# Performance work log

Hardware: AMD Instinct MI355X
Metric: run time of the kernel (lower is better)

The kernel has to match this reference:

```python
import jax, jax.numpy as jnp
import numpy as np
import math

SAMPLE_RATIO = 0.25
K = 5
EPS = 1e-6

def _cells(loc_orig, H, W):
    # map normalized [-1,1] coords to nearest grid cell index, as in tcformer token2map/map2token
    loc = jnp.clip(loc_orig, -1.0, 1.0)
    px = jnp.clip(jnp.round(0.5 * (loc[..., 0] + 1.0) * W - 0.5).astype(jnp.int32), 0, W - 1)
    py = jnp.clip(jnp.round(0.5 * (loc[..., 1] + 1.0) * H - 0.5).astype(jnp.int32), 0, H - 1)
    return py * W + px  # [B, N0]

def token2map(x, loc_orig, idx_agg, H, W):
    B, N, C = x.shape
    N0 = loc_orig.shape[1]
    cell = _cells(loc_orig, H, W)
    seg = (cell + jnp.arange(B)[:, None] * (H * W)).reshape(-1)
    feat = x[jnp.arange(B)[:, None], idx_agg]  # [B, N0, C] token feature per original point
    sums = jax.ops.segment_sum(feat.reshape(-1, C), seg, num_segments=B * H * W)
    cnt = jax.ops.segment_sum(jnp.ones((B * N0,), x.dtype), seg, num_segments=B * H * W)
    x_map = sums / (cnt[:, None] + EPS)  # per-cell mean over points hitting the cell
    return x_map.reshape(B, H, W, C).transpose(0, 3, 1, 2)

def map2token(x_map, N, loc_orig, idx_agg, agg_weight):
    B, C, H, W = x_map.shape
    cell = _cells(loc_orig, H, W)
    val = x_map.reshape(B, C, H * W).transpose(0, 2, 1)  # [B, HW, C]
    vpt = val[jnp.arange(B)[:, None], cell]              # [B, N0, C] map value at each point
    seg = (idx_agg + jnp.arange(B)[:, None] * N).reshape(-1)
    w = agg_weight.reshape(-1)
    wsum = jax.ops.segment_sum(w, seg, num_segments=B * N) + EPS
    ssum = jax.ops.segment_sum(vpt.reshape(-1, C) * w[:, None], seg, num_segments=B * N)
    return (ssum / wsum[:, None]).reshape(B, N, C)  # agg_weight-weighted mean per token

def token_cluster_merge(x, Ns, idx_agg, weight, k):
    B, N, C = x.shape
    # DPC-KNN clustering (index computation; mirrors torch.no_grad block)
    sq = jnp.sum(x * x, -1)
    d2 = jnp.clip(sq[:, :, None] + sq[:, None, :] - 2.0 * jnp.einsum('bnc,bmc->bnm', x, x), 0.0, None)
    dist = jnp.sqrt(d2) / (C ** 0.5)
    dnear = -jax.lax.top_k(-dist, k)[0]                  # k smallest distances (incl. self)
    density = jnp.exp(-jnp.mean(dnear * dnear, -1))
    mask = density[:, None, :] > density[:, :, None]
    dmax = jnp.max(dist.reshape(B, -1), -1)[:, None, None]
    parent_dist = jnp.min(jnp.where(mask, dist, dmax), -1)  # dist to nearest higher-density token
    score = parent_dist * density
    index_down = jax.lax.top_k(score, Ns)[1]             # [B, Ns] cluster centers
    idx_cluster = jnp.argmin(dist[jnp.arange(B)[:, None], index_down], axis=1)  # [B, N]
    idx_cluster = idx_cluster.at[jnp.arange(B)[:, None], index_down].set(jnp.arange(Ns)[None, :])
    # weighted merge of tokens into clusters
    seg = (idx_cluster + jnp.arange(B)[:, None] * Ns).reshape(-1)
    w = weight.reshape(-1)
    allw = jax.ops.segment_sum(w, seg, num_segments=B * Ns) + EPS
    norm_w = (w / allw[seg]).reshape(B, N)
    x_merged = jax.ops.segment_sum((x * norm_w[:, :, None]).reshape(-1, C), seg, num_segments=B * Ns).reshape(B, Ns, C)
    idx_agg_down = idx_cluster[jnp.arange(B)[:, None], idx_agg]      # compose index maps
    weight_t = norm_w[jnp.arange(B)[:, None], idx_agg][..., None]    # [B, N0, 1]
    return x_merged, idx_agg_down, weight_t

def _forward(x, loc_orig, idx_agg, agg_weight, idx_k_loc, H, W, conv_w, conv_b, skip_w, ln_g, ln_b, conf_w, conf_b):
    B, N, C = x.shape
    x_map = token2map(x, loc_orig, idx_agg, H, W)
    x_map = jax.lax.conv_general_dilated(x_map, conv_w, (2, 2), ((1, 1), (1, 1))) + conv_b[None, :, None, None]
    x_tok = map2token(x_map, N, loc_orig, idx_agg, agg_weight) + jnp.einsum('bnc,oc->bno', x, skip_w)
    mu = jnp.mean(x_tok, -1, keepdims=True)
    var = jnp.mean((x_tok - mu) ** 2, -1, keepdims=True)
    x_tok = (x_tok - mu) / jnp.sqrt(var + 1e-5) * ln_g + ln_b
    conf = jnp.einsum('bnc,oc->bno', x_tok, conf_w) + conf_b
    weight = jnp.exp(conf)
    Ns = max(math.ceil(N * SAMPLE_RATIO), 1)
    x_down, idx_agg_down, weight_t = token_cluster_merge(x_tok, Ns, idx_agg, weight, K)
    agg_weight_down = agg_weight * weight_t
    agg_weight_down = agg_weight_down / jnp.max(agg_weight_down, axis=1, keepdims=True)
    # down_block is an injected submodule; treated as identity passthrough here
    return x_down, idx_agg_down, agg_weight_down

def setup_inputs():
    key = jax.random.key(0)
    ks = jax.random.split(key, 8)
    B, N, C, N0, Cout = 8, 256, 256, 16384, 512
    return {
        'x': jax.random.normal(ks[0], (B, N, C), jnp.float32),
        'loc_orig': jax.random.uniform(ks[1], (B, N0, 2), jnp.float32, -1.0, 1.0),
        'idx_agg': jax.random.randint(ks[2], (B, N0), 0, N),
        'agg_weight': jax.random.uniform(ks[3], (B, N0, 1), jnp.float32, 0.1, 1.0),
        'idx_k_loc': jax.random.randint(ks[4], (B, N0, K), 0, N0),
        'H': 64, 'W': 64,
        'conv_w': jax.random.normal(ks[5], (Cout, C, 3, 3), jnp.float32) * 0.02,
        'conv_b': jnp.zeros((Cout,), jnp.float32),
        'skip_w': jax.random.normal(ks[6], (Cout, C), jnp.float32) * 0.02,
        'ln_g': jnp.ones((Cout,), jnp.float32),
        'ln_b': jnp.zeros((Cout,), jnp.float32),
        'conf_w': jax.random.normal(ks[7], (1, Cout), jnp.float32) * 0.02,
        'conf_b': jnp.zeros((1,), jnp.float32),
    }

def reference(x, loc_orig, idx_agg, agg_weight, idx_k_loc, H, W, conv_w, conv_b, skip_w, ln_g, ln_b, conf_w, conf_b):
    return _forward(x, loc_orig, idx_agg, agg_weight, idx_k_loc, H, W, conv_w, conv_b, skip_w, ln_g, ln_b, conf_w, conf_b)
```

## Files before the change

### kernel.cpp

```cpp
#include <hip/hip_runtime.h>
#include <math.h>

typedef unsigned long long ull;
typedef __attribute__((ext_vector_type(8))) short short8v;
typedef __attribute__((ext_vector_type(4))) float float4v;

#define NB   8
#define NTOK 256
#define CIN  256
#define NP   16384
#define NCO  512
#define HW64 4096
#define OHW  1024
#define NS   64
#define EPS  1e-6f
#define KC   2304
#define NKC  72

constexpr size_t OFF_SUMS = 0;
constexpr size_t OFF_CNT  = OFF_SUMS + (size_t)NB*HW64*CIN;
constexpr size_t OFF_AMAT = OFF_CNT  + (size_t)NB*HW64;
constexpr size_t OFF_ALLW = OFF_AMAT + (size_t)NB*NTOK*OHW;
constexpr size_t OFF_DMAX = OFF_ALLW + (size_t)NB*NS;
constexpr size_t OFF_MAXW = OFF_DMAX + NB;
constexpr size_t ZERO_END = OFF_MAXW + NB;
constexpr size_t OFF_WT   = ZERO_END;
constexpr size_t OFF_SKWT = OFF_WT   + (size_t)KC*NCO;
constexpr size_t OFF_Y    = OFF_SKWT + (size_t)CIN*NCO;
constexpr size_t OFF_C2   = OFF_Y    + (size_t)NB*OHW*NCO;
constexpr size_t OFF_WSUM = OFF_C2   + (size_t)NB*NTOK*NCO;
constexpr size_t OFF_XSKIP= OFF_WSUM + (size_t)NB*NTOK;
constexpr size_t OFF_XTOK = OFF_XSKIP+ (size_t)NB*NTOK*NCO;
constexpr size_t OFF_XPK  = OFF_XTOK + (size_t)NB*NTOK*NCO;
constexpr size_t OFF_WEXP = OFF_XPK  + (size_t)NB*NTOK*NCO;
constexpr size_t OFF_SQ   = OFF_WEXP + (size_t)NB*NTOK;
constexpr size_t OFF_DIST = OFF_SQ   + (size_t)NB*NTOK;
constexpr size_t OFF_DENS = OFF_DIST + (size_t)NB*NTOK*NTOK;
constexpr size_t OFF_SCORE= OFF_DENS + (size_t)NB*NTOK;
constexpr size_t OFF_IND  = OFF_SCORE+ (size_t)NB*NTOK;
constexpr size_t OFF_IDXCL= OFF_IND  + (size_t)NB*NS;
constexpr size_t OFF_NORMW= OFF_IDXCL+ (size_t)NB*NTOK;
constexpr size_t OFF_AWBUF= OFF_NORMW+ (size_t)NB*NTOK;
constexpr size_t OFF_XTPK = OFF_AWBUF+ (size_t)NB*NP;
constexpr size_t OFF_XTOKPK= OFF_Y;

__device__ __forceinline__ unsigned pack_hl(float x) {
    unsigned u = __float_as_uint(x);
    unsigned t = u + 0x7fffu + ((u >> 16) & 1u);
    unsigned hibits = t & 0xffff0000u;
    float lo = x - __uint_as_float(hibits);
    unsigned ul = __float_as_uint(lo);
    unsigned lt = ul + 0x7fffu + ((ul >> 16) & 1u);
    return hibits | (lt >> 16);
}
__device__ __forceinline__ unsigned f2bf(float f) {
    unsigned u = __float_as_uint(f);
    return (u + 0x7fffu + ((u >> 16) & 1u)) >> 16;
}
__device__ __forceinline__ unsigned hp2(unsigned w0, unsigned w1) {
    return __builtin_amdgcn_perm(w1, w0, 0x07060302u);
}
__device__ __forceinline__ unsigned lp2(unsigned w0, unsigned w1) {
    return __builtin_amdgcn_perm(w1, w0, 0x05040100u);
}

__global__ void hist(const float* __restrict__ loc, const int* __restrict__ idxagg,
                     const float* __restrict__ aggw,
                     int* __restrict__ cntmat, float* __restrict__ cnt,
                     float* __restrict__ amat) {
    int bp = blockIdx.x*256 + threadIdx.x;
    int b  = bp >> 14;
    float lx = loc[2*bp+0], ly = loc[2*bp+1];
    lx = fminf(fmaxf(lx, -1.f), 1.f);
    ly = fminf(fmaxf(ly, -1.f), 1.f);
    int px = (int)rintf((lx + 1.f)*32.f - 0.5f); px = min(max(px,0),63);
    int py = (int)rintf((ly + 1.f)*32.f - 0.5f); py = min(max(py,0),63);
    int cell = py*64 + px;
    int tok = idxagg[bp];
    atomicAdd(&cntmat[((size_t)(b*HW64 + cell))*NTOK + tok], 1);
    atomicAdd(&cnt[b*HW64 + cell], 1.0f);
    int qx = (int)rintf((lx + 1.f)*16.f - 0.5f); qx = min(max(qx,0),31);
    int qy = (int)rintf((ly + 1.f)*16.f - 0.5f); qy = min(max(qy,0),31);
    atomicAdd(&amat[((size_t)(b*NTOK + tok))*OHW + qy*32 + qx], aggw[bp]);
}

__global__ void prep_pack(const float* __restrict__ x, unsigned* __restrict__ xtpk,
                          unsigned* __restrict__ xpk,
                          const float* __restrict__ convw, uint4* __restrict__ wtf,
                          const float4* __restrict__ skipw, uint4* __restrict__ skwt) {
    int blk = blockIdx.x;
    if (blk < 2048) {
        int id = blk*256 + threadIdx.x;
        int tok = id & 255, cin = (id >> 8) & 255, b = id >> 16;
        unsigned pk = pack_hl(x[((size_t)(b*NTOK + tok))*CIN + cin]);
        xtpk[id] = pk;
        xpk[((size_t)(b*NTOK + tok))*CIN + cin] = pk;
    } else if (blk < 3200) {
        int tid = (blk - 2048)*256 + threadIdx.x;
        int lane = tid & 63;
        int r1 = tid >> 6;
        int h = r1 & 1;
        int r2 = r1 >> 1;
        int f = r2 & 3;
        int r3 = r2 >> 2;
        int kc = r3 % NKC, mt = r3 / NKC;
        int cout = mt*64 + f*16 + (lane & 15);
        int kb = kc*32 + (lane >> 4)*8;
        unsigned s[8];
        #pragma unroll
        for (int j = 0; j < 8; ++j) {
            int k = kb + j;
            int grp = k >> 8, cin = k & 255;
            unsigned w = pack_hl(convw[(size_t)cout*KC + cin*9 + grp]);
            s[j] = h ? (w & 0xffffu) : (w >> 16);
        }
        uint4 o;
        o.x = s[0] | (s[1]<<16); o.y = s[2] | (s[3]<<16);
        o.z = s[4] | (s[5]<<16); o.w = s[6] | (s[7]<<16);
        wtf[tid] = o;
    } else {
        size_t i = (size_t)(blk - 3200)*256 + threadIdx.x;
        float4 v = skipw[i];
        uint4 o;
        o.x = pack_hl(v.x); o.y = pack_hl(v.y); o.z = pack_hl(v.z); o.w = pack_hl(v.w);
        skwt[i] = o;
    }
}

__launch_bounds__(512)
__global__ void map_gemm(const int* __restrict__ A, const unsigned* __restrict__ B,
                         const float* __restrict__ cnt, unsigned* __restrict__ xmapu) {
    __shared__ __align__(16) unsigned short Ah[4096];
    __shared__ __align__(16) unsigned short Bh[8192], Bl[8192];
    int z = blockIdx.z, m0 = blockIdx.y*128;
    const int* Ab = A + ((size_t)z*HW64 + m0)*NTOK;
    const unsigned* Bb = B + (size_t)z*CIN*NTOK;
    int t = threadIdx.x, lane = t & 63;
    int w = t >> 6;
    int wm = w >> 2, wn = w & 3;
    int l15 = lane & 15, l4 = lane >> 4;
    int rowA = t & 127, kgA = t >> 7;
    int rowB = t & 255, kgB0 = (t >> 8)*2;
    const int* arow = Ab + (size_t)rowA*NTOK + kgA*8;
    const unsigned* brow = Bb + (size_t)rowB*NTOK + kgB0*8;
    int wbA = (rowA>>4)*512 + kgA*128 + (rowA&15)*8;
    int wbB = (rowB>>4)*512 + kgB0*128 + (rowB&15)*8;

    float4v acc[4][4] = {};
    int4 ia0, ia1;
    uint4 rb[2][2];
    auto loadA = [&](int kc) {
        const int* p = arow + kc*32;
        ia0 = *(const int4*)p; ia1 = *(const int4*)(p + 4);
    };
    auto loadB = [&](int kc) {
        #pragma unroll
        for (int s = 0; s < 2; ++s) {
            const unsigned* p = brow + kc*32 + s*8;
            rb[s][0] = *(const uint4*)p; rb[s][1] = *(const uint4*)(p + 4);
        }
    };
    loadA(0); loadB(0);

    for (int kc = 0; kc < 8; ++kc) {
        __syncthreads();
        uint4 h, l;
        h.x = f2bf((float)ia0.x) | (f2bf((float)ia0.y) << 16);
        h.y = f2bf((float)ia0.z) | (f2bf((float)ia0.w) << 16);
        h.z = f2bf((float)ia1.x) | (f2bf((float)ia1.y) << 16);
        h.w = f2bf((float)ia1.z) | (f2bf((float)ia1.w) << 16);
        *(uint4*)&Ah[wbA] = h;
        #pragma unroll
        for (int s = 0; s < 2; ++s) {
            uint4 u0 = rb[s][0], u1 = rb[s][1];
            h.x=hp2(u0.x,u0.y); h.y=hp2(u0.z,u0.w); h.z=hp2(u1.x,u1.y); h.w=hp2(u1.z,u1.w);
            l.x=lp2(u0.x,u0.y); l.y=lp2(u0.z,u0.w); l.z=lp2(u1.x,u1.y); l.w=lp2(u1.z,u1.w);
            *(uint4*)&Bh[wbB + s*128] = h; *(uint4*)&Bl[wbB + s*128] = l;
        }
        __syncthreads();
        if (kc < 7) { loadA(kc+1); loadB(kc+1); }

        short8v bh[4], bl[4];
        #pragma unroll
        for (int q = 0; q < 4; ++q) {
            int off = (wn*4 + q)*512 + l4*128 + l15*8;
            bh[q] = *(const short8v*)&Bh[off];
            bl[q] = *(const short8v*)&Bl[off];
        }
        #pragma unroll
        for (int p = 0; p < 4; ++p) {
            int off = (wm*4 + p)*512 + l4*128 + l15*8;
            short8v ah = *(const short8v*)&Ah[off];
            #pragma unroll
            for (int q = 0; q < 4; ++q) {
                acc[p][q] = __builtin_amdgcn_mfma_f32_16x16x32_bf16(ah, bh[q], acc[p][q], 0, 0, 0);
                acc[p][q] = __builtin_amdgcn_mfma_f32_16x16x32_bf16(ah, bl[q], acc[p][q], 0, 0, 0);
            }
        }
    }

    const float* cntb = cnt + (size_t)z*HW64;
    #pragma unroll
    for (int p = 0; p < 4; ++p) {
        int mb = m0 + wm*64 + p*16 + l4*4;
        #pragma unroll
        for (int q = 0; q < 4; ++q) {
            int n = wn*64 + q*16 + l15;
            #pragma unroll
            for (int r = 0; r < 4; ++r) {
                float v = acc[p][q][r] / (cntb[mb + r] + EPS);
                xmapu[((size_t)z*HW64 + mb + r)*CIN + n] = pack_hl(v);
            }
        }
    }
}

__launch_bounds__(256)
__global__ void conv_gemm(const unsigned* __restrict__ xmap, const uint4* __restrict__ wtf,
                          const float* __restrict__ convb, unsigned* __restrict__ ytp) {
    __shared__ __align__(16) unsigned short Ahi[2][4096], Alo[2][4096];
    int n0 = blockIdx.x * 128;
    int mt = blockIdx.y;
    int m0 = mt * 64;
    int t = threadIdx.x;
    int lane = t & 63, wid = t >> 6;
    int wm = wid >> 1, wn = wid & 1;
    int l15 = lane & 15, l4 = lane >> 4;

    int rowL = t & 127, kg = t >> 7;
    int posG = n0 + rowL;
    int bb = posG >> 10, rem = posG & 1023;
    int oy = rem >> 5, ox = rem & 31;

    int wbA0 = (rowL>>4)*512 + kg*128 + (rowL&15)*8;
    int wbA1 = wbA0 + 256;

    float4v acc[4][2] = {};
    uint4 aA0,aA1,aA2,aA3;
    uint4 aB0,aB1,aB2,aB3;

    auto addrA = [&](int kc, int* ok) -> const unsigned* {
        int grp = kc >> 3;
        int ky = grp/3, kx = grp - 3*ky;
        int iy = 2*oy - 1 + ky, ix = 2*ox - 1 + kx;
        *ok = ((unsigned)iy < 64u) && ((unsigned)ix < 64u);
        return xmap + ((((size_t)bb*64 + iy)*64 + ix)*256 + (kc&7)*32 + kg*8);
    };
    auto loadA_A = [&](int kc) {
        int ok; const unsigned* ap = addrA(kc, &ok);
        if (ok) {
            aA0 = *(const uint4*)ap;       aA1 = *(const uint4*)(ap + 4);
            aA2 = *(const uint4*)(ap + 16); aA3 = *(const uint4*)(ap + 20);
        } else { aA0 = make_uint4(0,0,0,0); aA1 = aA0; aA2 = aA0; aA3 = aA0; }
    };
    auto loadA_B = [&](int kc) {
        int ok; const unsigned* ap = addrA(kc, &ok);
        if (ok) {
            aB0 = *(const uint4*)ap;       aB1 = *(const uint4*)(ap + 4);
            aB2 = *(const uint4*)(ap + 16); aB3 = *(const uint4*)(ap + 20);
        } else { aB0 = make_uint4(0,0,0,0); aB1 = aB0; aB2 = aB0; aB3 = aB0; }
    };
    auto repack_A = [&](int buf) {
        uint4 h, l;
        h.x=hp2(aA0.x,aA0.y); h.y=hp2(aA0.z,aA0.w); h.z=hp2(aA1.x,aA1.y); h.w=hp2(aA1.z,aA1.w);
        l.x=lp2(aA0.x,aA0.y); l.y=lp2(aA0.z,aA0.w); l.z=lp2(aA1.x,aA1.y); l.w=lp2(aA1.z,aA1.w);
        *(uint4*)&Ahi[buf][wbA0] = h; *(uint4*)&Alo[buf][wbA0] = l;
        h.x=hp2(aA2.x,aA2.y); h.y=hp2(aA2.z,aA2.w); h.z=hp2(aA3.x,aA3.y); h.w=hp2(aA3.z,aA3.w);
        l.x=lp2(aA2.x,aA2.y); l.y=lp2(aA2.z,aA2.w); l.z=lp2(aA3.x,aA3.y); l.w=lp2(aA3.z,aA3.w);
        *(uint4*)&Ahi[buf][wbA1] = h; *(uint4*)&Alo[buf][wbA1] = l;
    };
    auto repack_B = [&](int buf) {
        uint4 h, l;
        h.x=hp2(aB0.x,aB0.y); h.y=hp2(aB0.z,aB0.w); h.z=hp2(aB1.x,aB1.y); h.w=hp2(aB1.z,aB1.w);
        l.x=lp2(aB0.x,aB0.y); l.y=lp2(aB0.z,aB0.w); l.z=lp2(aB1.x,aB1.y); l.w=lp2(aB1.z,aB1.w);
        *(uint4*)&Ahi[buf][wbA0] = h; *(uint4*)&Alo[buf][wbA0] = l;
        h.x=hp2(aB2.x,aB2.y); h.y=hp2(aB2.z,aB2.w); h.z=hp2(aB3.x,aB3.y); h.w=hp2(aB3.z,aB3.w);
        l.x=lp2(aB2.x,aB2.y); l.y=lp2(aB2.z,aB2.w); l.z=lp2(aB3.x,aB3.y); l.w=lp2(aB3.z,aB3.w);
        *(uint4*)&Ahi[buf][wbA1] = h; *(uint4*)&Alo[buf][wbA1] = l;
    };
    const uint4* wbase = wtf + ((size_t)(((mt*NKC)*4 + wn*2)*2))*64 + lane;

    short8v bhc[2], blc[2], bhn[2], bln[2];
    #pragma unroll
    for (int q = 0; q < 2; ++q) {
        bhc[q] = *(const short8v*)(wbase + q*128);
        blc[q] = *(const short8v*)(wbase + q*128 + 64);
    }
    loadA_B(0);
    repack_B(0);
    loadA_A(1);
    __syncthreads();
    int cur = 0;

    #define CONV_MFMA_BLOCK                                                            \
        _Pragma("unroll")                                                              \
        for (int p = 0; p < 4; ++p) {                                                  \
            int off = (wm*4 + p)*512 + l4*128 + l15*8;                                 \
            short8v ah = *(const short8v*)&Ahi[cur][off];                              \
            short8v al = *(const short8v*)&Alo[cur][off];                              \
            _Pragma("unroll")                                                          \
            for (int q = 0; q < 2; ++q) {                                              \
                acc[p][q] = __builtin_amdgcn_mfma_f32_16x16x32_bf16(ah, bhc[q], acc[p][q], 0, 0, 0); \
                acc[p][q] = __builtin_amdgcn_mfma_f32_16x16x32_bf16(ah, blc[q], acc[p][q], 0, 0, 0); \
                acc[p][q] = __builtin_amdgcn_mfma_f32_16x16x32_bf16(al, bhc[q], acc[p][q], 0, 0, 0); \
            }                                                                          \
        }

    for (int kc = 0; kc < NKC; kc += 2) {
        {
            const uint4* wb = wbase + (size_t)(kc+1)*512;
            #pragma unroll
            for (int q = 0; q < 2; ++q) {
                bhn[q] = *(const short8v*)(wb + q*128);
                bln[q] = *(const short8v*)(wb + q*128 + 64);
            }
        }
        if (kc + 2 < NKC) loadA_B(kc + 2);
        CONV_MFMA_BLOCK
        repack_A(cur ^ 1);
        #pragma unroll
        for (int q = 0; q < 2; ++q) { bhc[q] = bhn[q]; blc[q] = bln[q]; }
        __syncthreads();
        cur ^= 1;

        int k1 = kc + 1;
        if (k1 + 1 < NKC) {
            const uint4* wb = wbase + (size_t)(k1+1)*512;
            #pragma unroll
            for (int q = 0; q < 2; ++q) {
                bhn[q] = *(const short8v*)(wb + q*128);
                bln[q] = *(const short8v*)(wb + q*128 + 64);
            }
        }
        if (k1 + 2 < NKC) loadA_A(k1 + 2);
        CONV_MFMA_BLOCK
        if (k1 + 1 < NKC) {
            repack_B(cur ^ 1);
            #pragma unroll
            for (int q = 0; q < 2; ++q) { bhc[q] = bhn[q]; blc[q] = bln[q]; }
        }
        __syncthreads();
        cur ^= 1;
    }
    #undef CONV_MFMA_BLOCK

    int bbk = n0 >> 10;
    int pos0 = (n0 & 1023) + wm*64;
    #pragma unroll
    for (int p = 0; p < 4; ++p) {
        int posb = pos0 + p*16 + l4*4;
        #pragma unroll
        for (int q = 0; q < 2; ++q) {
            int col = m0 + wn*32 + q*16 + l15;
            float bv = convb[col];
            uint4 o;
            o.x = pack_hl(acc[p][q][0] + bv);
            o.y = pack_hl(acc[p][q][1] + bv);
            o.z = pack_hl(acc[p][q][2] + bv);
            o.w = pack_hl(acc[p][q][3] + bv);
            *(uint4*)&ytp[((size_t)(bbk*NCO + col))*OHW + posb] = o;
        }
    }
}

template<int MODE, int TM, int TN, int AF>
__launch_bounds__(256)
__global__ void gemm_pk(const void* __restrict__ Av, const unsigned* __restrict__ B,
                        float* __restrict__ C, int K, int N,
                        long sA, long sB, long sC,
                        const float* __restrict__ aux, unsigned* __restrict__ dmaxU) {
    constexpr int NA = TM/64, NBs = TN/64;
    constexpr int WSM = TM/64;
    constexpr int WSN = 4/WSM;
    constexpr int TWM = TM/WSM, TWN = TN/WSN;
    constexpr int P = TWM/16, Q = TWN/16;
    __shared__ __align__(16) unsigned short Ahi[TM*32], Alo[TM*32];
    __shared__ __align__(16) unsigned short Bhi[TN*32], Blo[TN*32];
    int z = blockIdx.z;
    const unsigned* Ab = (const unsigned*)Av + (size_t)z*sA;
    const unsigned* Bb = B + (size_t)z*sB;
    float* Cb = C + (size_t)z*sC;
    int n0 = blockIdx.x*TN, m0 = blockIdx.y*TM;
    int t = threadIdx.x;
    int lane = t & 63, wid = t >> 6;
    int wm = (WSM==2) ? (wid >> 1) : 0;
    int wn = (WSM==2) ? (wid & 1)  : wid;
    int l15 = lane & 15, l4 = lane >> 4;

    int rowA = t & (TM-1), kgA = t / TM;
    int rowB = t & (TN-1), kgB = t / TN;
    const unsigned* arow = Ab + (size_t)(m0 + rowA)*K + kgA*8;
    const unsigned* brw  = Bb + (size_t)(n0 + rowB)*K + kgB*8;
    int wbA = (rowA>>4)*512 + kgA*128 + (rowA&15)*8;
    int wbB = (rowB>>4)*512 + kgB*128 + (rowB&15)*8;

    float4v acc[P][Q] = {};
    uint4 ra[NA][2], rb[NBs][2];
    auto loadA = [&](int kc) {
        #pragma unroll
        for (int s = 0; s < NA; ++s) {
            const unsigned* p = arow + (size_t)kc*32 + s*16;
            ra[s][0] = *(const uint4*)p; ra[s][1] = *(const uint4*)(p + 4);
        }
    };
    auto loadB = [&](int kc) {
        #pragma unroll
        for (int s = 0; s < NBs; ++s) {
            const unsigned* p = brw + (size_t)kc*32 + s*16;
            rb[s][0] = *(const uint4*)p; rb[s][1] = *(const uint4*)(p + 4);
        }
    };
    loadA(0); loadB(0);
    int nkc = K >> 5;

    for (int kc = 0; kc < nkc; ++kc) {
        __syncthreads();
        uint4 h, l;
        #pragma unroll
        for (int s = 0; s < NA; ++s) {
            uint4 u0 = ra[s][0], u1 = ra[s][1];
            if (AF == 0) {
                h.x=hp2(u0.x,u0.y); h.y=hp2(u0.z,u0.w); h.z=hp2(u1.x,u1.y); h.w=hp2(u1.z,u1.w);
                l.x=lp2(u0.x,u0.y); l.y=lp2(u0.z,u0.w); l.z=lp2(u1.x,u1.y); l.w=lp2(u1.z,u1.w);
            } else {
                unsigned pk0 = pack_hl(__uint_as_float(u0.x)), pk1 = pack_hl(__uint_as_float(u0.y));
                unsigned pk2 = pack_hl(__uint_as_float(u0.z)), pk3 = pack_hl(__uint_as_float(u0.w));
                unsigned pk4 = pack_hl(__uint_as_float(u1.x)), pk5 = pack_hl(__uint_as_float(u1.y));
                unsigned pk6 = pack_hl(__uint_as_float(u1.z)), pk7 = pack_hl(__uint_as_float(u1.w));
                h.x = (pk0>>16) | (pk1 & 0xffff0000u); h.y = (pk2>>16) | (pk3 & 0xffff0000u);
                h.z = (pk4>>16) | (pk5 & 0xffff0000u); h.w = (pk6>>16) | (pk7 & 0xffff0000u);
                l.x = (pk0&0xffffu) | (pk1<<16); l.y = (pk2&0xffffu) | (pk3<<16);
                l.z = (pk4&0xffffu) | (pk5<<16); l.w = (pk6&0xffffu) | (pk7<<16);
            }
            *(uint4*)&Ahi[wbA + s*256] = h; *(uint4*)&Alo[wbA + s*256] = l;
        }
        #pragma unroll
        for (int s = 0; s < NBs; ++s) {
            uint4 u0 = rb[s][0], u1 = rb[s][1];
            h.x=hp2(u0.x,u0.y); h.y=hp2(u0.z,u0.w); h.z=hp2(u1.x,u1.y); h.w=hp2(u1.z,u1.w);
            l.x=lp2(u0.x,u0.y); l.y=lp2(u0.z,u0.w); l.z=lp2(u1.x,u1.y); l.w=lp2(u1.z,u1.w);
            *(uint4*)&Bhi[wbB + s*256] = h; *(uint4*)&Blo[wbB + s*256] = l;
        }
        __syncthreads();
        if (kc + 1 < nkc) { loadA(kc+1); loadB(kc+1); }

        short8v bh[Q], bl[Q];
        #pragma unroll
        for (int q = 0; q < Q; ++q) {
            int off = (wn*Q + q)*512 + l4*128 + l15*8;
            bh[q] = *(const short8v*)&Bhi[off];
            bl[q] = *(const short8v*)&Blo[off];
        }
        #pragma unroll
        for (int p = 0; p < P; ++p) {
            int off = (wm*P + p)*512 + l4*128 + l15*8;
            short8v ah = *(const short8v*)&Ahi[off];
            short8v al = *(const short8v*)&Alo[off];
            #pragma unroll
            for (int q = 0; q < Q; ++q) {
                acc[p][q] = __builtin_amdgcn_mfma_f32_16x16x32_bf16(ah, bh[q], acc[p][q], 0, 0, 0);
                acc[p][q] = __builtin_amdgcn_mfma_f32_16x16x32_bf16(ah, bl[q], acc[p][q], 0, 0, 0);
                acc[p][q] = __builtin_amdgcn_mfma_f32_16x16x32_bf16(al, bh[q], acc[p][q], 0, 0, 0);
            }
        }
    }

    if (MODE == 0) {
        #pragma unroll
        for (int p = 0; p < P; ++p) {
            int mb = m0 + wm*TWM + p*16 + l4*4;
            #pragma unroll
            for (int q = 0; q < Q; ++q) {
                int n = n0 + wn*TWN + q*16 + l15;
                #pragma unroll
                for (int r = 0; r < 4; ++r)
                    Cb[(size_t)(mb + r)*N + n] = acc[p][q][r];
            }
        }
    } else {
        const float inv = 1.0f / sqrtf(512.0f);
        const float* sqb = aux + (size_t)z*NTOK;
        float tmax = 0.f;
        #pragma unroll
        for (int p = 0; p < P; ++p) {
            int mb = m0 + wm*TWM + p*16 + l4*4;
            #pragma unroll
            for (int q = 0; q < Q; ++q) {
                int n = n0 + wn*TWN + q*16 + l15;
                float sn = sqb[n];
                #pragma unroll
                for (int r = 0; r < 4; ++r) {
                    float d2 = sqb[mb + r] + sn - 2.0f*acc[p][q][r];
                    float d = sqrtf(fmaxf(d2, 0.0f)) * inv;
                    Cb[(size_t)(mb + r)*N + n] = d;
                    tmax = fmaxf(tmax, d);
                }
            }
        }
        __shared__ float redm[4];
        #pragma unroll
        for (int off = 32; off; off >>= 1) tmax = fmaxf(tmax, __shfl_xor(tmax, off, 64));
        if (lane == 0) redm[wid] = tmax;
        __syncthreads();
        if (t == 0) {
            float m = fmaxf(fmaxf(redm[0], redm[1]), fmaxf(redm[2], redm[3]));
            atomicMax(dmaxU + z, __float_as_uint(m));
        }
    }
}

__global__ void wsum_rows(const float* __restrict__ amat, float* __restrict__ wsum) {
    int row = blockIdx.x*4 + (threadIdx.x >> 6);
    int lane = threadIdx.x & 63;
    const float* ar = amat + (size_t)row*OHW;
    float s = 0.f;
    #pragma unroll
    for (int r = 0; r < 16; ++r) s += ar[lane + 64*r];
    #pragma unroll
    for (int off = 32; off; off >>= 1) s += __shfl_xor(s, off, 64);
    if (lane == 0) wsum[row] = s;
}

__device__ __forceinline__ float block_sum256(float v, float* red) {
    #pragma unroll
    for (int off = 32; off; off >>= 1) v += __shfl_xor(v, off, 64);
    __syncthreads();
    if ((threadIdx.x & 63) == 0) red[threadIdx.x >> 6] = v;
    __syncthreads();
    return red[0] + red[1] + red[2] + red[3];
}

__global__ void ln_conf(const float* __restrict__ C2, const float* __restrict__ wsum,
                        const float* __restrict__ xskip, const float* __restrict__ g,
                        const float* __restrict__ be, const float* __restrict__ confw,
                        const float* __restrict__ confb, float* __restrict__ xtok,
                        unsigned* __restrict__ xtokpk,
                        float* __restrict__ wexp, float* __restrict__ sqv) {
    __shared__ float red[4];
    int row = blockIdx.x, t = threadIdx.x;
    float ws = wsum[row] + EPS;
    size_t base = (size_t)row*NCO;
    float v0 = C2[base + t]       / ws + xskip[base + t];
    float v1 = C2[base + t + 256] / ws + xskip[base + t + 256];
    float mu  = block_sum256(v0 + v1, red) / 512.0f;
    float d0 = v0 - mu, d1 = v1 - mu;
    float var = block_sum256(d0*d0 + d1*d1, red) / 512.0f;
    float sv = sqrtf(var + 1e-5f);
    float x0 = d0/sv * g[t]       + be[t];
    float x1 = d1/sv * g[t + 256] + be[t + 256];
    xtok[base + t] = x0;
    xtok[base + t + 256] = x1;
    xtokpk[base + t] = pack_hl(x0);
    xtokpk[base + t + 256] = pack_hl(x1);
    float cs = block_sum256(x0*confw[t] + x1*confw[t + 256], red);
    float qs = block_sum256(x0*x0 + x1*x1, red);
    if (t == 0) {
        wexp[row] = expf(cs + confb[0]);
        sqv[row]  = qs;
    }
}

__global__ void knn_dens(const float* __restrict__ dist, float* __restrict__ dens) {
    int row = blockIdx.x*4 + (threadIdx.x >> 6);
    int lane = threadIdx.x & 63;
    const float* dr = dist + (size_t)row*NTOK;
    float v0 = dr[lane], v1 = dr[lane+64], v2 = dr[lane+128], v3 = dr[lane+192];
    float acc = 0.f;
    #pragma unroll
    for (int it = 0; it < 5; ++it) {
        float lm = fminf(fminf(v0, v1), fminf(v2, v3));
        float gm = lm;
        #pragma unroll
        for (int off = 32; off; off >>= 1) gm = fminf(gm, __shfl_xor(gm, off, 64));
        acc += gm*gm;
        ull ball = __ballot(lm == gm);
        int first = __ffsll(ball) - 1;
        if (lane == first) {
            if      (v0 == gm) v0 = 1e30f;
            else if (v1 == gm) v1 = 1e30f;
            else if (v2 == gm) v2 = 1e30f;
            else               v3 = 1e30f;
        }
    }
    if (lane == 0) dens[row] = expf(-(acc/5.0f));
}

__global__ void parent_score(const float* __restrict__ dist, const float* __restrict__ dens,
                             const unsigned* __restrict__ dmaxU, float* __restrict__ score) {
    int row = blockIdx.x*4 + (threadIdx.x >> 6);
    int lane = threadIdx.x & 63;
    int b = row >> 8;
    float di = dens[row];
    float dm = __uint_as_float(dmaxU[b]);
    const float* dr = dist + (size_t)row*NTOK;
    const float* db = dens + (size_t)b*NTOK;
    float pd = dm;
    #pragma unroll
    for (int r = 0; r < 4; ++r) {
        int j = lane + 64*r;
        pd = fminf(pd, (db[j] > di) ? dr[j] : dm);
    }
    #pragma unroll
    for (int off = 32; off; off >>= 1) pd = fminf(pd, __shfl_xor(pd, off, 64));
    if (lane == 0) score[row] = pd * di;
}

__global__ void topk64(const float* __restrict__ score, int* __restrict__ ind) {
    int b = blockIdx.x, lane = threadIdx.x;
    const float* sb = score + b*NTOK;
    ull k0, k1, k2, k3;
    {
        unsigned i0 = lane, i1 = lane+64, i2 = lane+128, i3 = lane+192;
        k0 = ((ull)(__float_as_uint(sb[i0]) + 1u) << 32) | (unsigned)(4095 - i0);
        k1 = ((ull)(__float_as_uint(sb[i1]) + 1u) << 32) | (unsigned)(4095 - i1);
        k2 = ((ull)(__float_as_uint(sb[i2]) + 1u) << 32) | (unsigned)(4095 - i2);
        k3 = ((ull)(__float_as_uint(sb[i3]) + 1u) << 32) | (unsigned)(4095 - i3);
    }
    for (int it = 0; it < 64; ++it) {
        ull lm = k0;
        if (k1 > lm) lm = k1;
        if (k2 > lm) lm = k2;
        if (k3 > lm) lm = k3;
        ull gm = lm;
        #pragma unroll
        for (int off = 32; off; off >>= 1) {
            ull o = __shfl_xor(gm, off, 64);
            if (o > gm) gm = o;
        }
        if (lane == 0) ind[b*NS + it] = 4095 - (int)(gm & 0xffffffffull);
        if      (k0 == gm) k0 = 0;
        else if (k1 == gm) k1 = 0;
        else if (k2 == gm) k2 = 0;
        else if (k3 == gm) k3 = 0;
    }
}

__global__ void assign_k(const float* __restrict__ dist, const int* __restrict__ ind,
                         int* __restrict__ idxcl) {
    int row = blockIdx.x*4 + (threadIdx.x >> 6);
    int lane = threadIdx.x & 63;
    int b = row >> 8, i = row & 255;
    int center = ind[b*NS + lane];
    float d = dist[((size_t)(b*NTOK + center))*NTOK + i];
    ull key = ((ull)__float_as_uint(d) << 32) | (unsigned)lane;
    #pragma unroll
    for (int off = 32; off; off >>= 1) {
        ull o = __shfl_xor(key, off, 64);
        if (o < key) key = o;
    }
    if (lane == 0) idxcl[row] = (int)(key & 0xffffffffull);
}

__global__ void finalize_cl(const int* __restrict__ ind, const float* __restrict__ wexp,
                            int* __restrict__ idxcl, float* __restrict__ normw) {
    __shared__ float allwL[NS];
    int b = blockIdx.x, t = threadIdx.x;
    if (t < NS) {
        idxcl[b*NTOK + ind[b*NS + t]] = t;
        allwL[t] = 0.f;
    }
    __syncthreads();
    int cl = idxcl[b*NTOK + t];
    float we = wexp[b*NTOK + t];
    atomicAdd(&allwL[cl], we);
    __syncthreads();
    normw[b*NTOK + t] = we / (allwL[cl] + EPS);
}

__global__ void merge_k(const float* __restrict__ xtok, const int* __restrict__ idxcl,
                        const float* __restrict__ normw, float* __restrict__ xout) {
    int row = blockIdx.x, t = threadIdx.x;
    int b = row >> 8;
    int cl = idxcl[row];
    float nw = normw[row];
    float* o = xout + ((size_t)(b*NS + cl))*NCO;
    const float* xr = xtok + (size_t)row*NCO;
    atomicAdd(&o[t],       xr[t]       * nw);
    atomicAdd(&o[t + 256], xr[t + 256] * nw);
}

__global__ void out_idx_aw(const int* __restrict__ idxagg, const float* __restrict__ aggw,
                           const int* __restrict__ idxcl, const float* __restrict__ normw,
                           float* __restrict__ dout, float* __restrict__ awbuf,
                           unsigned* __restrict__ maxw) {
    __shared__ float red[4];
    int bp = blockIdx.x*256 + threadIdx.x;
    int b = bp >> 14;
    int tok = idxagg[bp];
    int cl = idxcl[b*NTOK + tok];
    dout[(size_t)NB*NS*NCO + bp] = (float)cl;
    float aw = aggw[bp] * normw[b*NTOK + tok];
    awbuf[bp] = aw;
    float m = aw;
    #pragma unroll
    for (int off = 32; off; off >>= 1) m = fmaxf(m, __shfl_xor(m, off, 64));
    if ((threadIdx.x & 63) == 0) red[threadIdx.x >> 6] = m;
    __syncthreads();
    if (threadIdx.x == 0) {
        float mm = fmaxf(fmaxf(red[0], red[1]), fmaxf(red[2], red[3]));
        atomicMax(&maxw[b], __float_as_uint(mm));
    }
}

__global__ void aw_final(const float* __restrict__ awbuf, const float* __restrict__ maxw,
                         float* __restrict__ dout) {
    int bp = blockIdx.x*256 + threadIdx.x;
    int b = bp >> 14;
    dout[(size_t)NB*NS*NCO + (size_t)NB*NP + bp] = awbuf[bp] / maxw[b];
}

extern "C" void kernel_launch(void* const* d_in, const int* in_sizes, int n_in,
                              void* d_out, int out_size, void* d_ws, size_t ws_size,
                              hipStream_t stream) {
    const float* x      = (const float*)d_in[0];
    const float* loc    = (const float*)d_in[1];
    const int*   idxagg = (const int*)  d_in[2];
    const float* aggw   = (const float*)d_in[3];
    const float* convw  = (const float*)d_in[7];
    const float* convb  = (const float*)d_in[8];
    const float* skipw  = (const float*)d_in[9];
    const float* lng    = (const float*)d_in[10];
    const float* lnb    = (const float*)d_in[11];
    const float* confw  = (const float*)d_in[12];
    const float* confb  = (const float*)d_in[13];

    float* ws = (float*)d_ws;
    float* dout = (float*)d_out;

    (void)hipMemsetAsync(ws, 0, ZERO_END*sizeof(float), stream);
    (void)hipMemsetAsync(dout, 0, (size_t)NB*NS*NCO*sizeof(float), stream);

    hist<<<dim3(NB*NP/256), 256, 0, stream>>>(loc, idxagg, aggw,
                                              (int*)(ws + OFF_SUMS), ws + OFF_CNT, ws + OFF_AMAT);
    prep_pack<<<dim3(3328), 256, 0, stream>>>(x, (unsigned*)(ws + OFF_XTPK),
                                              (unsigned*)(ws + OFF_XPK),
                                              convw, (uint4*)(ws + OFF_WT),
                                              (const float4*)skipw, (uint4*)(ws + OFF_SKWT));

    map_gemm<<<dim3(1, 32, 8), 512, 0, stream>>>((const int*)(ws + OFF_SUMS),
                                                 (const unsigned*)(ws + OFF_XTPK),
                                                 ws + OFF_CNT,
                                                 (unsigned*)(ws + OFF_SUMS));

    conv_gemm<<<dim3(64, 8), 256, 0, stream>>>((const unsigned*)(ws + OFF_SUMS),
                                               (const uint4*)(ws + OFF_WT), convb,
                                               (unsigned*)(ws + OFF_Y));

    wsum_rows<<<dim3(NB*NTOK/4), 256, 0, stream>>>(ws + OFF_AMAT, ws + OFF_WSUM);
    gemm_pk<0,64,64,1><<<dim3(8, 4, 8), 256, 0, stream>>>((const void*)(ws + OFF_AMAT),
                                                  (const unsigned*)(ws + OFF_Y),
                                                  ws + OFF_C2, OHW, NCO,
                                                  (long)NTOK*OHW, (long)NCO*OHW, (long)NTOK*NCO,
                                                  nullptr, nullptr);
    gemm_pk<0,64,64,0><<<dim3(8, 32, 1), 256, 0, stream>>>((const void*)(ws + OFF_XPK),
                                                   (const unsigned*)(ws + OFF_SKWT),
                                                   ws + OFF_XSKIP, CIN, NCO, 0, 0, 0,
                                                   nullptr, nullptr);

    ln_conf<<<dim3(NB*NTOK), 256, 0, stream>>>(ws + OFF_C2, ws + OFF_WSUM, ws + OFF_XSKIP,
                                               lng, lnb, confw, confb,
                                               ws + OFF_XTOK, (unsigned*)(ws + OFF_XTOKPK),
                                               ws + OFF_WEXP, ws + OFF_SQ);

    gemm_pk<1,64,64,0><<<dim3(4, 4, 8), 256, 0, stream>>>((const void*)(ws + OFF_XTOKPK),
                                                  (const unsigned*)(ws + OFF_XTOKPK),
                                                  ws + OFF_DIST, NCO, NTOK,
                                                  (long)NTOK*NCO, (long)NTOK*NCO, (long)NTOK*NTOK,
                                                  ws + OFF_SQ, (unsigned*)(ws + OFF_DMAX));

    knn_dens<<<dim3(NB*NTOK/4), 256, 0, stream>>>(ws + OFF_DIST, ws + OFF_DENS);
    parent_score<<<dim3(NB*NTOK/4), 256, 0, stream>>>(ws + OFF_DIST, ws + OFF_DENS,
                                                      (const unsigned*)(ws + OFF_DMAX), ws + OFF_SCORE);
    topk64<<<dim3(NB), 64, 0, stream>>>(ws + OFF_SCORE, (int*)(ws + OFF_IND));
    assign_k<<<dim3(NB*NTOK/4), 256, 0, stream>>>(ws + OFF_DIST, (const int*)(ws + OFF_IND),
                                                  (int*)(ws + OFF_IDXCL));
    finalize_cl<<<dim3(NB), 256, 0, stream>>>((const int*)(ws + OFF_IND), ws + OFF_WEXP,
                                              (int*)(ws + OFF_IDXCL), ws + OFF_NORMW);

    merge_k<<<dim3(NB*NTOK), 256, 0, stream>>>(ws + OFF_XTOK, (const int*)(ws + OFF_IDXCL),
                                               ws + OFF_NORMW, dout);
    out_idx_aw<<<dim3(NB*NP/256), 256, 0, stream>>>(idxagg, aggw, (const int*)(ws + OFF_IDXCL),
                                                    ws + OFF_NORMW, dout, ws + OFF_AWBUF,
                                                    (unsigned*)(ws + OFF_MAXW));
    aw_final<<<dim3(NB*NP/256), 256, 0, stream>>>(ws + OFF_AWBUF, (const float*)(ws + OFF_MAXW), dout);
}
```

Before: 282.1 us.

## Pack histogram counts into 16-bit pairs and double conv K-stage size

The per-cell token count matrix is stored as two packed 16-bit counters per word. It lives in the Y buffer region, so the count matrix and the memset that clears it are half the size, and map_gemm reads half the bytes for A. The conv GEMM now stages 64 channels per LDS buffer instead of 32, which halves the number of barriers and repack rounds per K loop at the cost of twice the shared memory and more staging registers. Packed counters assume no cell/token pair exceeds 65535 hits, which holds here since each batch has at most 16384 points.

Result: slower. 296.7 us (+5.2%).

```diff
diff --git a/kernel.cpp b/kernel.cpp
--- a/kernel.cpp
+++ b/kernel.cpp
@@ -16,6 +16,7 @@
 #define EPS  1e-6f
 #define KC   2304
 #define NKC  72
+#define NPAIR 36
 
 constexpr size_t OFF_SUMS = 0;
 constexpr size_t OFF_CNT  = OFF_SUMS + (size_t)NB*HW64*CIN;
@@ -66,7 +67,7 @@
 
 __global__ void hist(const float* __restrict__ loc, const int* __restrict__ idxagg,
                      const float* __restrict__ aggw,
-                     int* __restrict__ cntmat, float* __restrict__ cnt,
+                     unsigned* __restrict__ cnt16, float* __restrict__ cnt,
                      float* __restrict__ amat) {
     int bp = blockIdx.x*256 + threadIdx.x;
     int b  = bp >> 14;
@@ -77,7 +78,7 @@
     int py = (int)rintf((ly + 1.f)*32.f - 0.5f); py = min(max(py,0),63);
     int cell = py*64 + px;
     int tok = idxagg[bp];
-    atomicAdd(&cntmat[((size_t)(b*HW64 + cell))*NTOK + tok], 1);
+    atomicAdd(&cnt16[((size_t)(b*HW64 + cell))*128 + (tok >> 1)], 1u << ((tok & 1)*16));
     atomicAdd(&cnt[b*HW64 + cell], 1.0f);
     int qx = (int)rintf((lx + 1.f)*16.f - 0.5f); qx = min(max(qx,0),31);
     int qy = (int)rintf((ly + 1.f)*16.f - 0.5f); qy = min(max(qy,0),31);
@@ -128,12 +129,12 @@
 }
 
 __launch_bounds__(512)
-__global__ void map_gemm(const int* __restrict__ A, const unsigned* __restrict__ B,
+__global__ void map_gemm(const unsigned* __restrict__ A16, const unsigned* __restrict__ B,
                          const float* __restrict__ cnt, unsigned* __restrict__ xmapu) {
     __shared__ __align__(16) unsigned short Ah[4096];
     __shared__ __align__(16) unsigned short Bh[8192], Bl[8192];
     int z = blockIdx.z, m0 = blockIdx.y*128;
-    const int* Ab = A + ((size_t)z*HW64 + m0)*NTOK;
+    const unsigned* Ab = A16 + ((size_t)z*HW64 + m0)*128;
     const unsigned* Bb = B + (size_t)z*CIN*NTOK;
     int t = threadIdx.x, lane = t & 63;
     int w = t >> 6;
@@ -141,17 +142,16 @@
     int l15 = lane & 15, l4 = lane >> 4;
     int rowA = t & 127, kgA = t >> 7;
     int rowB = t & 255, kgB0 = (t >> 8)*2;
-    const int* arow = Ab + (size_t)rowA*NTOK + kgA*8;
+    const unsigned* arow = Ab + (size_t)rowA*128 + kgA*4;
     const unsigned* brow = Bb + (size_t)rowB*NTOK + kgB0*8;
     int wbA = (rowA>>4)*512 + kgA*128 + (rowA&15)*8;
     int wbB = (rowB>>4)*512 + kgB0*128 + (rowB&15)*8;
 
     float4v acc[4][4] = {};
-    int4 ia0, ia1;
+    uint4 ia;
     uint4 rb[2][2];
     auto loadA = [&](int kc) {
-        const int* p = arow + kc*32;
-        ia0 = *(const int4*)p; ia1 = *(const int4*)(p + 4);
+        ia = *(const uint4*)(arow + kc*16);
     };
     auto loadB = [&](int kc) {
         #pragma unroll
@@ -165,10 +165,10 @@
     for (int kc = 0; kc < 8; ++kc) {
         __syncthreads();
         uint4 h, l;
-        h.x = f2bf((float)ia0.x) | (f2bf((float)ia0.y) << 16);
-        h.y = f2bf((float)ia0.z) | (f2bf((float)ia0.w) << 16);
-        h.z = f2bf((float)ia1.x) | (f2bf((float)ia1.y) << 16);
-        h.w = f2bf((float)ia1.z) | (f2bf((float)ia1.w) << 16);
+        h.x = f2bf((float)(ia.x & 0xffffu)) | (f2bf((float)(ia.x >> 16)) << 16);
+        h.y = f2bf((float)(ia.y & 0xffffu)) | (f2bf((float)(ia.y >> 16)) << 16);
+        h.z = f2bf((float)(ia.z & 0xffffu)) | (f2bf((float)(ia.z >> 16)) << 16);
+        h.w = f2bf((float)(ia.w & 0xffffu)) | (f2bf((float)(ia.w >> 16)) << 16);
         *(uint4*)&Ah[wbA] = h;
         #pragma unroll
         for (int s = 0; s < 2; ++s) {
@@ -218,7 +218,7 @@
 __launch_bounds__(256)
 __global__ void conv_gemm(const unsigned* __restrict__ xmap, const uint4* __restrict__ wtf,
                           const float* __restrict__ convb, unsigned* __restrict__ ytp) {
-    __shared__ __align__(16) unsigned short Ahi[2][4096], Alo[2][4096];
+    __shared__ __align__(16) unsigned short Ahi[2][8192], Alo[2][8192];
     int n0 = blockIdx.x * 128;
     int mt = blockIdx.y;
     int m0 = mt * 64;
@@ -231,118 +231,125 @@
     int posG = n0 + rowL;
     int bb = posG >> 10, rem = posG & 1023;
     int oy = rem >> 5, ox = rem & 31;
-
-    int wbA0 = (rowL>>4)*512 + kg*128 + (rowL&15)*8;
-    int wbA1 = wbA0 + 256;
+    int wbBase = (rowL>>4)*1024 + (kg*4)*128 + (rowL&15)*8;
 
     float4v acc[4][2] = {};
-    uint4 aA0,aA1,aA2,aA3;
-    uint4 aB0,aB1,aB2,aB3;
-
-    auto addrA = [&](int kc, int* ok) -> const unsigned* {
-        int grp = kc >> 3;
+    uint4 rA[8], rB[8];
+
+    auto stageA = [&](int pr) {
+        int grp = pr >> 2;
         int ky = grp/3, kx = grp - 3*ky;
         int iy = 2*oy - 1 + ky, ix = 2*ox - 1 + kx;
-        *ok = ((unsigned)iy < 64u) && ((unsigned)ix < 64u);
-        return xmap + ((((size_t)bb*64 + iy)*64 + ix)*256 + (kc&7)*32 + kg*8);
+        if ((unsigned)iy < 64u && (unsigned)ix < 64u) {
+            const unsigned* ap = xmap + ((((size_t)bb*64 + iy)*64 + ix)*256 + (pr&3)*64 + kg*32);
+            #pragma unroll
+            for (int s = 0; s < 8; ++s) rA[s] = *(const uint4*)(ap + s*4);
+        } else {
+            #pragma unroll
+            for (int s = 0; s < 8; ++s) rA[s] = make_uint4(0,0,0,0);
+        }
     };
-    auto loadA_A = [&](int kc) {
-        int ok; const unsigned* ap = addrA(kc, &ok);
-        if (ok) {
-            aA0 = *(const uint4*)ap;       aA1 = *(const uint4*)(ap + 4);
-            aA2 = *(const uint4*)(ap + 16); aA3 = *(const uint4*)(ap + 20);
-        } else { aA0 = make_uint4(0,0,0,0); aA1 = aA0; aA2 = aA0; aA3 = aA0; }
+    auto stageB = [&](int pr) {
+        int grp = pr >> 2;
+        int ky = grp/3, kx = grp - 3*ky;
+        int iy = 2*oy - 1 + ky, ix = 2*ox - 1 + kx;
+        if ((unsigned)iy < 64u && (unsigned)ix < 64u) {
+            const unsigned* ap = xmap + ((((size_t)bb*64 + iy)*64 + ix)*256 + (pr&3)*64 + kg*32);
+            #pragma unroll
+            for (int s = 0; s < 8; ++s) rB[s] = *(const uint4*)(ap + s*4);
+        } else {
+            #pragma unroll
+            for (int s = 0; s < 8; ++s) rB[s] = make_uint4(0,0,0,0);
+        }
     };
-    auto loadA_B = [&](int kc) {
-        int ok; const unsigned* ap = addrA(kc, &ok);
-        if (ok) {
-            aB0 = *(const uint4*)ap;       aB1 = *(const uint4*)(ap + 4);
-            aB2 = *(const uint4*)(ap + 16); aB3 = *(const uint4*)(ap + 20);
-        } else { aB0 = make_uint4(0,0,0,0); aB1 = aB0; aB2 = aB0; aB3 = aB0; }
+    auto repackA = [&](int buf) {
+        #pragma unroll
+        for (int s = 0; s < 4; ++s) {
+            uint4 u0 = rA[2*s], u1 = rA[2*s+1], h, l;
+            h.x=hp2(u0.x,u0.y); h.y=hp2(u0.z,u0.w); h.z=hp2(u1.x,u1.y); h.w=hp2(u1.z,u1.w);
+            l.x=lp2(u0.x,u0.y); l.y=lp2(u0.z,u0.w); l.z=lp2(u1.x,u1.y); l.w=lp2(u1.z,u1.w);
+            *(uint4*)&Ahi[buf][wbBase + s*128] = h;
+            *(uint4*)&Alo[buf][wbBase + s*128] = l;
+        }
     };
-    auto repack_A = [&](int buf) {
-        uint4 h, l;
-        h.x=hp2(aA0.x,aA0.y); h.y=hp2(aA0.z,aA0.w); h.z=hp2(aA1.x,aA1.y); h.w=hp2(aA1.z,aA1.w);
-        l.x=lp2(aA0.x,aA0.y); l.y=lp2(aA0.z,aA0.w); l.z=lp2(aA1.x,aA1.y); l.w=lp2(aA1.z,aA1.w);
-        *(uint4*)&Ahi[buf][wbA0] = h; *(uint4*)&Alo[buf][wbA0] = l;
-        h.x=hp2(aA2.x,aA2.y); h.y=hp2(aA2.z,aA2.w); h.z=hp2(aA3.x,aA3.y); h.w=hp2(aA3.z,aA3.w);
-        l.x=lp2(aA2.x,aA2.y); l.y=lp2(aA2.z,aA2.w); l.z=lp2(aA3.x,aA3.y); l.w=lp2(aA3.z,aA3.w);
-        *(uint4*)&Ahi[buf][wbA1] = h; *(uint4*)&Alo[buf][wbA1] = l;
-    };
-    auto repack_B = [&](int buf) {
-        uint4 h, l;
-        h.x=hp2(aB0.x,aB0.y); h.y=hp2(aB0.z,aB0.w); h.z=hp2(aB1.x,aB1.y); h.w=hp2(aB1.z,aB1.w);
-        l.x=lp2(aB0.x,aB0.y); l.y=lp2(aB0.z,aB0.w); l.z=lp2(aB1.x,aB1.y); l.w=lp2(aB1.z,aB1.w);
-        *(uint4*)&Ahi[buf][wbA0] = h; *(uint4*)&Alo[buf][wbA0] = l;
-        h.x=hp2(aB2.x,aB2.y); h.y=hp2(aB2.z,aB2.w); h.z=hp2(aB3.x,aB3.y); h.w=hp2(aB3.z,aB3.w);
-        l.x=lp2(aB2.x,aB2.y); l.y=lp2(aB2.z,aB2.w); l.z=lp2(aB3.x,aB3.y); l.w=lp2(aB3.z,aB3.w);
-        *(uint4*)&Ahi[buf][wbA1] = h; *(uint4*)&Alo[buf][wbA1] = l;
+    auto repackB = [&](int buf) {
+        #pragma unroll
+        for (int s = 0; s < 4; ++s) {
+            uint4 u0 = rB[2*s], u1 = rB[2*s+1], h, l;
+            h.x=hp2(u0.x,u0.y); h.y=hp2(u0.z,u0.w); h.z=hp2(u1.x,u1.y); h.w=hp2(u1.z,u1.w);
+            l.x=lp2(u0.x,u0.y); l.y=lp2(u0.z,u0.w); l.z=lp2(u1.x,u1.y); l.w=lp2(u1.z,u1.w);
+            *(uint4*)&Ahi[buf][wbBase + s*128] = h;
+            *(uint4*)&Alo[buf][wbBase + s*128] = l;
+        }
     };
     const uint4* wbase = wtf + ((size_t)(((mt*NKC)*4 + wn*2)*2))*64 + lane;
 
     short8v bhc[2], blc[2], bhn[2], bln[2];
+    #define LOADB(kc)                                                   \
+        {                                                               \
+            const uint4* wb = wbase + (size_t)(kc)*512;                 \
+            _Pragma("unroll")                                           \
+            for (int q = 0; q < 2; ++q) {                               \
+                bhn[q] = *(const short8v*)(wb + q*128);                 \
+                bln[q] = *(const short8v*)(wb + q*128 + 64);            \
+            }                                                           \
+        }
+    #define BSWAP                                                       \
+        _Pragma("unroll")                                               \
+        for (int q = 0; q < 2; ++q) { bhc[q] = bhn[q]; blc[q] = bln[q]; }
+
+    #define CONV_MFMA(J)                                                                    \
+        _Pragma("unroll")                                                                   \
+        for (int p = 0; p < 4; ++p) {                                                       \
+            int off = (wm*4 + p)*1024 + ((J)*4 + l4)*128 + l15*8;                           \
+            short8v ah = *(const short8v*)&Ahi[cur][off];                                   \
+            short8v al = *(const short8v*)&Alo[cur][off];                                   \
+            _Pragma("unroll")                                                               \
+            for (int q = 0; q < 2; ++q) {                                                   \
+                acc[p][q] = __builtin_amdgcn_mfma_f32_16x16x32_bf16(ah, bhc[q], acc[p][q], 0, 0, 0); \
+                acc[p][q] = __builtin_amdgcn_mfma_f32_16x16x32_bf16(ah, blc[q], acc[p][q], 0, 0, 0); \
+                acc[p][q] = __builtin_amdgcn_mfma_f32_16x16x32_bf16(al, bhc[q], acc[p][q], 0, 0, 0); \
+            }                                                                               \
+        }
+
+    stageB(0);
+    repackB(0);
     #pragma unroll
     for (int q = 0; q < 2; ++q) {
         bhc[q] = *(const short8v*)(wbase + q*128);
         blc[q] = *(const short8v*)(wbase + q*128 + 64);
     }
-    loadA_B(0);
-    repack_B(0);
-    loadA_A(1);
+    stageA(1);
     __syncthreads();
     int cur = 0;
 
-    #define CONV_MFMA_BLOCK                                                            \
-        _Pragma("unroll")                                                              \
-        for (int p = 0; p < 4; ++p) {                                                  \
-            int off = (wm*4 + p)*512 + l4*128 + l15*8;                                 \
-            short8v ah = *(const short8v*)&Ahi[cur][off];                              \
-            short8v al = *(const short8v*)&Alo[cur][off];                              \
-            _Pragma("unroll")                                                          \
-            for (int q = 0; q < 2; ++q) {                                              \
-                acc[p][q] = __builtin_amdgcn_mfma_f32_16x16x32_bf16(ah, bhc[q], acc[p][q], 0, 0, 0); \
-                acc[p][q] = __builtin_amdgcn_mfma_f32_16x16x32_bf16(ah, blc[q], acc[p][q], 0, 0, 0); \
-                acc[p][q] = __builtin_amdgcn_mfma_f32_16x16x32_bf16(al, bhc[q], acc[p][q], 0, 0, 0); \
-            }                                                                          \
-        }
-
-    for (int kc = 0; kc < NKC; kc += 2) {
-        {
-            const uint4* wb = wbase + (size_t)(kc+1)*512;
-            #pragma unroll
-            for (int q = 0; q < 2; ++q) {
-                bhn[q] = *(const short8v*)(wb + q*128);
-                bln[q] = *(const short8v*)(wb + q*128 + 64);
-            }
-        }
-        if (kc + 2 < NKC) loadA_B(kc + 2);
-        CONV_MFMA_BLOCK
-        repack_A(cur ^ 1);
-        #pragma unroll
-        for (int q = 0; q < 2; ++q) { bhc[q] = bhn[q]; blc[q] = bln[q]; }
+    for (int pr = 0; pr < NPAIR; pr += 2) {
+        LOADB(2*pr + 1);
+        if (pr + 2 < NPAIR) stageB(pr + 2);
+        CONV_MFMA(0)
+        BSWAP
+        LOADB(2*pr + 2);
+        CONV_MFMA(1)
+        repackA(cur ^ 1);
+        BSWAP
         __syncthreads();
         cur ^= 1;
 
-        int k1 = kc + 1;
-        if (k1 + 1 < NKC) {
-            const uint4* wb = wbase + (size_t)(k1+1)*512;
-            #pragma unroll
-            for (int q = 0; q < 2; ++q) {
-                bhn[q] = *(const short8v*)(wb + q*128);
-                bln[q] = *(const short8v*)(wb + q*128 + 64);
-            }
-        }
-        if (k1 + 2 < NKC) loadA_A(k1 + 2);
-        CONV_MFMA_BLOCK
-        if (k1 + 1 < NKC) {
-            repack_B(cur ^ 1);
-            #pragma unroll
-            for (int q = 0; q < 2; ++q) { bhc[q] = bhn[q]; blc[q] = bln[q]; }
-        }
+        int p1 = pr + 1;
+        LOADB(2*p1 + 1);
+        if (p1 + 2 < NPAIR) stageA(p1 + 2);
+        CONV_MFMA(0)
+        BSWAP
+        if (2*p1 + 2 < NKC) LOADB(2*p1 + 2);
+        CONV_MFMA(1)
+        if (p1 + 1 < NPAIR) repackB(cur ^ 1);
+        if (2*p1 + 2 < NKC) { BSWAP }
         __syncthreads();
         cur ^= 1;
     }
-    #undef CONV_MFMA_BLOCK
+    #undef CONV_MFMA
+    #undef LOADB
+    #undef BSWAP
 
     int bbk = n0 >> 10;
     int pos0 = (n0 & 1023) + wm*64;
@@ -727,17 +734,18 @@
     float* ws = (float*)d_ws;
     float* dout = (float*)d_out;
 
-    (void)hipMemsetAsync(ws, 0, ZERO_END*sizeof(float), stream);
+    (void)hipMemsetAsync(ws + OFF_CNT, 0, (ZERO_END - OFF_CNT)*sizeof(float), stream);
+    (void)hipMemsetAsync(ws + OFF_Y, 0, (size_t)NB*OHW*NCO*sizeof(float), stream);
     (void)hipMemsetAsync(dout, 0, (size_t)NB*NS*NCO*sizeof(float), stream);
 
     hist<<<dim3(NB*NP/256), 256, 0, stream>>>(loc, idxagg, aggw,
-                                              (int*)(ws + OFF_SUMS), ws + OFF_CNT, ws + OFF_AMAT);
+                                              (unsigned*)(ws + OFF_Y), ws + OFF_CNT, ws + OFF_AMAT);
     prep_pack<<<dim3(3328), 256, 0, stream>>>(x, (unsigned*)(ws + OFF_XTPK),
                                               (unsigned*)(ws + OFF_XPK),
                                               convw, (uint4*)(ws + OFF_WT),
                                               (const float4*)skipw, (uint4*)(ws + OFF_SKWT));
 
-    map_gemm<<<dim3(1, 32, 8), 512, 0, stream>>>((const int*)(ws + OFF_SUMS),
+    map_gemm<<<dim3(1, 32, 8), 512, 0, stream>>>((const unsigned*)(ws + OFF_Y),
                                                  (const unsigned*)(ws + OFF_XTPK),
                                                  ws + OFF_CNT,
                                                  (unsigned*)(ws + OFF_SUMS));
```
